# Kernel optimization log

Measured on AMD Instinct MI355X. Metric: run time of the kernel, lower is better.

## Reference

```python
import jax, jax.numpy as jnp
import numpy as np

B, S, D = 64, 1024, 64
NEG = -1e9


def setup_inputs() -> dict:
    key = jax.random.key(0)
    kq, kk, kv, kp = jax.random.split(key, 4)
    q = jax.random.normal(kq, (B, S, D), dtype=jnp.float32)
    k = jax.random.normal(kk, (B, S, D), dtype=jnp.float32)
    v = jax.random.normal(kv, (B, S, D), dtype=jnp.float32)
    prior_info = jax.random.normal(kp, (B, S, S), dtype=jnp.float32)
    # causal mask (True = masked), broadcast over batch
    causal = jnp.triu(jnp.ones((S, S), dtype=bool), k=1)
    mask = jnp.broadcast_to(causal, (B, S, S))
    return {"q": q, "k": k, "v": v, "mask": mask, "prior_info": prior_info}


def reference(q, k, v, mask, prior_info):
    # attn = q @ k^T / sqrt(d)
    attn = jnp.einsum("bqd,bkd->bqk", q, k)
    attn = attn / jnp.sqrt(jnp.asarray(D, dtype=attn.dtype))
    attn = jnp.where(mask, NEG, attn)
    prior = jnp.where(mask, NEG, prior_info)
    z = jax.nn.sigmoid(attn + prior)
    attn = z * attn + (1.0 - z) * prior
    attn = jax.nn.softmax(attn, axis=2)
    out = jnp.einsum("bqk,bkd->bqd", attn, v)
    return (out, attn)
```

## Files before the change

kernel.cpp:

```cpp
#include <hip/hip_runtime.h>
#include <math.h>

#define BB 64
#define SS 1024
#define DD 64
#define QB 32
#define THREADS 512

typedef __attribute__((ext_vector_type(8))) short short8;
typedef __attribute__((ext_vector_type(4))) float f32x4;

#define SWZ(row, byte) (((row) << 7) + (((((byte) >> 4) ^ ((row) & 7)) << 4) | ((byte) & 15)))

__device__ __forceinline__ unsigned short f2bf(float f) {
    union { float f; unsigned int u; } v; v.f = f;
    unsigned int r = (v.u + 0x7FFFu + ((v.u >> 16) & 1u)) >> 16;
    return (unsigned short)r;
}

__device__ __forceinline__ void gload16(const void* g, void* l) {
    __builtin_amdgcn_global_load_lds(
        (const __attribute__((address_space(1))) void*)g,
        (__attribute__((address_space(3))) void*)l, 16, 0, 0);
}

__global__ __launch_bounds__(256) void pre_convert(
    const float* __restrict__ qg, const float* __restrict__ kg,
    const float* __restrict__ vg, char* __restrict__ ws)
{
    __shared__ float sV[64][69];
    char* Kb = ws;
    char* Vt = ws + 8u * 1024u * 1024u;
    char* Qb = ws + 16u * 1024u * 1024u;
    const int bid = blockIdx.x, tid = threadIdx.x;

    if (bid < 1024) {
        const float* src = kg + ((size_t)(bid >> 4) * SS + (bid & 15) * 64) * DD;
        char* dst = Kb + (size_t)bid * 8192;
        #pragma unroll
        for (int u = 0; u < 4; ++u) {
            int idx = tid + u * 256, row = idx >> 4, c4 = idx & 15;
            f32x4 v = *(const f32x4*)(src + row * DD + c4 * 4);
            unsigned lo, hi;
            asm("v_cvt_pk_bf16_f32 %0, %1, %2" : "=v"(lo) : "v"(v.x), "v"(v.y));
            asm("v_cvt_pk_bf16_f32 %0, %1, %2" : "=v"(hi) : "v"(v.z), "v"(v.w));
            *(uint2*)(dst + SWZ(row, c4 * 8)) = make_uint2(lo, hi);
        }
    } else if (bid < 2048) {
        const int vb = bid - 1024;
        const float* src = vg + ((size_t)(vb >> 4) * SS + (vb & 15) * 64) * DD;
        #pragma unroll
        for (int u = 0; u < 4; ++u) {
            int idx = tid + u * 256, row = idx >> 4, c4 = idx & 15;
            f32x4 v = *(const f32x4*)(src + row * DD + c4 * 4);
            sV[row][c4 * 4 + 0] = v.x; sV[row][c4 * 4 + 1] = v.y;
            sV[row][c4 * 4 + 2] = v.z; sV[row][c4 * 4 + 3] = v.w;
        }
        __syncthreads();
        char* dst = Vt + (size_t)vb * 8192;
        const int d = tid >> 2, k0 = (tid & 3) * 16;
        union { short8 s; unsigned short u[8]; } w0, w1;
        #pragma unroll
        for (int i = 0; i < 8; ++i) {
            w0.u[i] = f2bf(sV[k0 + i][d]);
            w1.u[i] = f2bf(sV[k0 + 8 + i][d]);
        }
        *(short8*)(dst + SWZ(d, k0 * 2))      = w0.s;
        *(short8*)(dst + SWZ(d, k0 * 2 + 16)) = w1.s;
    } else {
        const int qb = bid - 2048;
        const float* src = qg + ((size_t)(qb >> 4) * SS + (qb & 15) * 64) * DD;
        char* dst = Qb + (size_t)qb * 8192;
        #pragma unroll
        for (int u = 0; u < 4; ++u) {
            int idx = tid + u * 256, row = idx >> 4, c4 = idx & 15;
            f32x4 v = *(const f32x4*)(src + row * DD + c4 * 4);
            float x0 = v.x * 0.125f, x1 = v.y * 0.125f;
            float x2 = v.z * 0.125f, x3 = v.w * 0.125f;
            unsigned lo, hi;
            asm("v_cvt_pk_bf16_f32 %0, %1, %2" : "=v"(lo) : "v"(x0), "v"(x1));
            asm("v_cvt_pk_bf16_f32 %0, %1, %2" : "=v"(hi) : "v"(x2), "v"(x3));
            *(uint2*)(dst + (row >> 5) * 4096 + SWZ(row & 31, c4 * 8)) = make_uint2(lo, hi);
        }
    }
}

__global__ __launch_bounds__(THREADS, 3) void attn_main(
    const char* __restrict__ ws, const float* __restrict__ prior,
    float* __restrict__ outg, float* __restrict__ attng)
{
    __shared__ char bufK[2][8192];
    __shared__ char bufV[3][8192];
    __shared__ char sP[2][4096];
    __shared__ float sRedP[QB][4];
    __shared__ float sRedT[QB];

    const int tid = threadIdx.x, lane = tid & 63, wid = tid >> 6;
    const int wr = wid >> 2, wc = wid & 3, lr = lane & 15, lg = lane >> 4;

    const int hw = (int)blockIdx.x;
    const int logical = ((hw & 7) << 8) | (hw >> 3);
    const int b  = logical >> 5;
    const int tq = 31 - (logical & 31);
    const int q0 = tq * QB;
    const int KT = (q0 + QB + 63) >> 6;

    const char* Kb = ws + (size_t)(b * 16) * 8192;
    const char* Vt = ws + 8u * 1024u * 1024u + (size_t)(b * 16) * 8192;
    const char* Qt = ws + 16u * 1024u * 1024u + (size_t)(b * 32 + tq) * 4096;

    short8 afr0 = *(const short8*)(Qt + SWZ(wr * 16 + lr, lg * 16));
    short8 afr1 = *(const short8*)(Qt + SWZ(wr * 16 + lr, 64 + lg * 16));

    const float* priB = prior + (size_t)b * SS * SS;
    const int rg0 = q0 + wr * 16 + lg * 4;
    const float* prow = priB + (size_t)rg0 * SS + (wc * 16 + lr);

    unsigned Zlo[16], Zhi[16];
    #pragma unroll
    for (int t = 0; t < 16; ++t) { Zlo[t] = 0u; Zhi[t] = 0u; }
    f32x4 oacc = (f32x4){0.f, 0.f, 0.f, 0.f};

    float prA[3][4];

    {
        gload16(Kb + tid * 16, (char*)&bufK[0][0] + tid * 16);
        gload16(Vt + tid * 16, (char*)&bufV[0][0] + tid * 16);
        prA[0][0] = prow[0]; prA[0][1] = prow[SS];
        prA[0][2] = prow[2 * SS]; prA[0][3] = prow[3 * SS];
        const int tp = (1 < KT) ? 1 : (KT - 1);
        const float* pp = prow + tp * 64;
        prA[1][0] = pp[0]; prA[1][1] = pp[SS];
        prA[1][2] = pp[2 * SS]; prA[1][3] = pp[3 * SS];
    }

    #pragma unroll
    for (int t = 0; t < 16; ++t) {
        if (t < KT) {
            __builtin_amdgcn_sched_barrier(0);
            asm volatile("s_waitcnt vmcnt(4) lgkmcnt(0)" ::: "memory");
            __builtin_amdgcn_sched_barrier(0);
            __builtin_amdgcn_s_barrier();
            __builtin_amdgcn_sched_barrier(0);

            {
                const int tn = (t + 1 < KT) ? (t + 1) : (KT - 1);
                gload16(Kb + (size_t)tn * 8192 + tid * 16,
                        (char*)&bufK[(t + 1) & 1][0] + tid * 16);
                gload16(Vt + (size_t)tn * 8192 + tid * 16,
                        (char*)&bufV[(t + 1) % 3][0] + tid * 16);
                const int tp = (t + 2 < KT) ? (t + 2) : (KT - 1);
                const float* pp = prow + tp * 64;
                prA[(t + 2) % 3][0] = pp[0];
                prA[(t + 2) % 3][1] = pp[SS];
                prA[(t + 2) % 3][2] = pp[2 * SS];
                prA[(t + 2) % 3][3] = pp[3 * SS];
            }

            const char* kb = &bufK[t & 1][0];
            short8 b0 = *(const short8*)(kb + SWZ(wc * 16 + lr, lg * 16));
            short8 b1 = *(const short8*)(kb + SWZ(wc * 16 + lr, 64 + lg * 16));
            f32x4 c = (f32x4){0.f, 0.f, 0.f, 0.f};
            c = __builtin_amdgcn_mfma_f32_16x16x32_bf16(afr0, b0, c, 0, 0, 0);
            c = __builtin_amdgcn_mfma_f32_16x16x32_bf16(afr1, b1, c, 0, 0, 0);

            if (t > 0) {
                const char* pb = &sP[(t - 1) & 1][0];
                const char* vb = &bufV[(t - 1) % 3][0];
                short8 pa0 = *(const short8*)(pb + SWZ(wr * 16 + lr, lg * 16));
                short8 pa1 = *(const short8*)(pb + SWZ(wr * 16 + lr, 64 + lg * 16));
                short8 vb0 = *(const short8*)(vb + SWZ(wc * 16 + lr, lg * 16));
                short8 vb1 = *(const short8*)(vb + SWZ(wc * 16 + lr, 64 + lg * 16));
                oacc = __builtin_amdgcn_mfma_f32_16x16x32_bf16(pa0, vb0, oacc, 0, 0, 0);
                oacc = __builtin_amdgcn_mfma_f32_16x16x32_bf16(pa1, vb1, oacc, 0, 0, 0);
            }

            const int colg = t * 64 + wc * 16 + lr;
            float e0, e1, e2, e3;
            {
                float ee[4];
                #pragma unroll
                for (int j = 0; j < 4; ++j) {
                    bool act = (colg <= rg0 + j);
                    float s = c[j];
                    float pv = prA[t % 3][j];
                    float z = 1.f / (1.f + __expf(-(s + pv)));
                    float m = pv + z * (s - pv);
                    ee[j] = act ? __expf(m) : 0.f;
                }
                e0 = ee[0]; e1 = ee[1]; e2 = ee[2]; e3 = ee[3];
            }

            unsigned X, Y;
            asm("v_cvt_pk_bf16_f32 %0, %1, %2" : "=v"(X) : "v"(e0), "v"(e1));
            asm("v_cvt_pk_bf16_f32 %0, %1, %2" : "=v"(Y) : "v"(e2), "v"(e3));
            unsigned Xp = (unsigned)__shfl_xor((int)X, 1);
            unsigned Yp = (unsigned)__shfl_xor((int)Y, 1);
            const bool codd = (lane & 1);
            unsigned nX = codd ? ((Xp >> 16) | (X & 0xffff0000u))
                               : ((X & 0xffffu) | (Xp << 16));
            unsigned nY = codd ? ((Yp >> 16) | (Y & 0xffff0000u))
                               : ((Y & 0xffffu) | (Yp << 16));
            unsigned X2 = (unsigned)__shfl_xor((int)nX, 2);
            unsigned Y2 = (unsigned)__shfl_xor((int)nY, 2);
            const bool chi = (lane & 2);
            unsigned Z0 = chi ? Y2 : nX;
            unsigned Z1 = chi ? nY : X2;
            Zlo[t] = Z0; Zhi[t] = Z1;

            const int c_ = lr & 3, a_ = lr >> 2;
            *(uint2*)(&sP[t & 1][0] + SWZ(wr * 16 + lg * 4 + c_, wc * 32 + a_ * 8)) =
                make_uint2(Z0, Z1);
        }
    }

    __builtin_amdgcn_sched_barrier(0);
    asm volatile("s_waitcnt lgkmcnt(0)" ::: "memory");
    __builtin_amdgcn_sched_barrier(0);
    __builtin_amdgcn_s_barrier();
    __builtin_amdgcn_sched_barrier(0);
    {
        const char* pb = &sP[(KT - 1) & 1][0];
        const char* vb = &bufV[(KT - 1) % 3][0];
        short8 pa0 = *(const short8*)(pb + SWZ(wr * 16 + lr, lg * 16));
        short8 pa1 = *(const short8*)(pb + SWZ(wr * 16 + lr, 64 + lg * 16));
        short8 vb0 = *(const short8*)(vb + SWZ(wc * 16 + lr, lg * 16));
        short8 vb1 = *(const short8*)(vb + SWZ(wc * 16 + lr, 64 + lg * 16));
        oacc = __builtin_amdgcn_mfma_f32_16x16x32_bf16(pa0, vb0, oacc, 0, 0, 0);
        oacc = __builtin_amdgcn_mfma_f32_16x16x32_bf16(pa1, vb1, oacc, 0, 0, 0);
    }

    const int c_ = lr & 3, a_ = lr >> 2;
    const int rL = wr * 16 + lg * 4 + c_;
    float sum4 = 0.f;
    #pragma unroll
    for (int t = 0; t < 16; ++t) {
        sum4 += __uint_as_float(Zlo[t] << 16);
        sum4 += __uint_as_float(Zlo[t] & 0xffff0000u);
        sum4 += __uint_as_float(Zhi[t] << 16);
        sum4 += __uint_as_float(Zhi[t] & 0xffff0000u);
    }
    sum4 += __shfl_xor(sum4, 4);
    sum4 += __shfl_xor(sum4, 8);
    if (a_ == 0) sRedP[rL][wc] = sum4;
    __syncthreads();
    if (tid < QB) {
        float tot = sRedP[tid][0] + sRedP[tid][1] + sRedP[tid][2] + sRedP[tid][3];
        sRedT[tid] = 1.f / tot;
    }
    __syncthreads();

    const float invT = sRedT[rL];
    float* arow = attng + ((size_t)b * SS + q0 + rL) * SS + wc * 16 + a_ * 4;
    #pragma unroll
    for (int t = 0; t < 16; ++t) {
        f32x4 vals;
        if (t < KT) {
            vals.x = __uint_as_float(Zlo[t] << 16) * invT;
            vals.y = __uint_as_float(Zlo[t] & 0xffff0000u) * invT;
            vals.z = __uint_as_float(Zhi[t] << 16) * invT;
            vals.w = __uint_as_float(Zhi[t] & 0xffff0000u) * invT;
        } else {
            vals = (f32x4){0.f, 0.f, 0.f, 0.f};
        }
        *(f32x4*)(arow + t * 64) = vals;
    }
    #pragma unroll
    for (int j = 0; j < 4; ++j) {
        float iv = sRedT[wr * 16 + lg * 4 + j];
        outg[((size_t)b * SS + rg0 + j) * DD + wc * 16 + lr] = oacc[j] * iv;
    }
}

#define KTILE 64
#define NTMAX 16
__device__ __forceinline__ int swzf(int row, int byte_in_row) {
    int chunk = (byte_in_row >> 4) ^ (row & 7);
    return row * 128 + chunk * 16 + (byte_in_row & 15);
}
__global__ __launch_bounds__(THREADS, 4) void attn_fallback(
    const float* __restrict__ qg, const float* __restrict__ kg,
    const float* __restrict__ vg, const float* __restrict__ prior,
    float* __restrict__ outg, float* __restrict__ attng)
{
    __shared__ char sQ[QB * 128];
    __shared__ char sKV[2][KTILE * 128];
    __shared__ char sPf[QB * 128];
    __shared__ float sRedA[QB][4];
    __shared__ float sRedB[QB][4];

    const int tid = threadIdx.x, lane = tid & 63, wid = tid >> 6;
    const int wr = wid >> 2, wc = wid & 3, lr = lane & 15, lg = lane >> 4;
    const int hw = (int)blockIdx.x;
    const int logical = ((hw & 7) << 8) | (hw >> 3);
    const int b = logical >> 5, tq = logical & 31;
    const int q0 = tq * QB;
    const int KT = (q0 + QB + KTILE - 1) / KTILE;
    const int rowg0 = q0 + wr * 16 + lg * 4;

    {
        int row = tid >> 4, c4 = tid & 15;
        f32x4 v = *(const f32x4*)(qg + ((size_t)b * SS + q0 + row) * DD + c4 * 4);
        ushort4 h = make_ushort4(f2bf(v.x), f2bf(v.y), f2bf(v.z), f2bf(v.w));
        *(ushort4*)(sQ + swzf(row, c4 * 8)) = h;
    }
    auto stageK = [&](const float* base, char* buf, int kt) {
        #pragma unroll
        for (int i = 0; i < 2; ++i) {
            int idx = tid + i * THREADS, row = idx >> 4, c4 = idx & 15;
            f32x4 v = *(const f32x4*)(base + ((size_t)b * SS + kt * KTILE + row) * DD + c4 * 4);
            ushort4 h = make_ushort4(f2bf(v.x), f2bf(v.y), f2bf(v.z), f2bf(v.w));
            *(ushort4*)(buf + swzf(row, c4 * 8)) = h;
        }
    };
    f32x4 acc[NTMAX];
    #pragma unroll
    for (int t = 0; t < NTMAX; ++t) acc[t] = (f32x4){0.f, 0.f, 0.f, 0.f};
    stageK(kg, sKV[0], 0);
    __syncthreads();
    short8 afr0 = *(const short8*)(sQ + swzf(wr * 16 + lr, lg * 16));
    short8 afr1 = *(const short8*)(sQ + swzf(wr * 16 + lr, 64 + lg * 16));
    const float* priB = prior + (size_t)b * SS * SS;
    #pragma unroll
    for (int t = 0; t < NTMAX; ++t) {
        if (t >= KT) continue;
        if (t + 1 < KT) stageK(kg, sKV[(t + 1) & 1], t + 1);
        const char* kb = sKV[t & 1];
        short8 b0 = *(const short8*)(kb + swzf(wc * 16 + lr, lg * 16));
        short8 b1 = *(const short8*)(kb + swzf(wc * 16 + lr, 64 + lg * 16));
        f32x4 c = acc[t];
        c = __builtin_amdgcn_mfma_f32_16x16x32_bf16(afr0, b0, c, 0, 0, 0);
        c = __builtin_amdgcn_mfma_f32_16x16x32_bf16(afr1, b1, c, 0, 0, 0);
        const int colg = t * KTILE + wc * 16 + lr;
        #pragma unroll
        for (int j = 0; j < 4; ++j) {
            int rg = rowg0 + j;
            bool act = (colg <= rg);
            float s = c[j] * 0.125f;
            float pv = act ? priB[(size_t)rg * SS + colg] : 0.f;
            float z = 1.f / (1.f + __expf(-(s + pv)));
            c[j] = act ? (pv + z * (s - pv)) : -1e9f;
        }
        acc[t] = c;
        __syncthreads();
    }
    float mj[4], sj[4], invj[4];
    #pragma unroll
    for (int j = 0; j < 4; ++j) {
        float m = -INFINITY;
        #pragma unroll
        for (int t = 0; t < NTMAX; ++t) if (t < KT) m = fmaxf(m, acc[t][j]);
        #pragma unroll
        for (int o = 1; o < 16; o <<= 1) m = fmaxf(m, __shfl_xor(m, o));
        mj[j] = m;
    }
    if (lr == 0) {
        #pragma unroll
        for (int j = 0; j < 4; ++j) sRedA[wr * 16 + lg * 4 + j][wc] = mj[j];
    }
    __syncthreads();
    #pragma unroll
    for (int j = 0; j < 4; ++j) {
        f32x4 r = *(const f32x4*)sRedA[wr * 16 + lg * 4 + j];
        mj[j] = fmaxf(fmaxf(r.x, r.y), fmaxf(r.z, r.w));
        sj[j] = 0.f;
    }
    #pragma unroll
    for (int t = 0; t < NTMAX; ++t) {
        if (t >= KT) continue;
        f32x4 c = acc[t];
        #pragma unroll
        for (int j = 0; j < 4; ++j) { c[j] = __expf(c[j] - mj[j]); sj[j] += c[j]; }
        acc[t] = c;
    }
    #pragma unroll
    for (int j = 0; j < 4; ++j) {
        float s = sj[j];
        #pragma unroll
        for (int o = 1; o < 16; o <<= 1) s += __shfl_xor(s, o);
        sj[j] = s;
    }
    if (lr == 0) {
        #pragma unroll
        for (int j = 0; j < 4; ++j) sRedB[wr * 16 + lg * 4 + j][wc] = sj[j];
    }
    __syncthreads();
    #pragma unroll
    for (int j = 0; j < 4; ++j) {
        f32x4 r = *(const f32x4*)sRedB[wr * 16 + lg * 4 + j];
        invj[j] = 1.f / (r.x + r.y + r.z + r.w);
    }
    #pragma unroll
    for (int t = 0; t < NTMAX; ++t) {
        const int colg = t * KTILE + wc * 16 + lr;
        #pragma unroll
        for (int j = 0; j < 4; ++j) {
            float p = 0.f;
            if (t < KT) p = acc[t][j] * invj[j];
            attng[((size_t)b * SS + rowg0 + j) * SS + colg] = p;
        }
        if (t < KT) {
            f32x4 c = acc[t];
            #pragma unroll
            for (int j = 0; j < 4; ++j) c[j] *= invj[j];
            acc[t] = c;
        }
    }
    f32x4 oacc = (f32x4){0.f, 0.f, 0.f, 0.f};
    #pragma unroll
    for (int t = 0; t < NTMAX; ++t) {
        if (t >= KT) continue;
        __syncthreads();
        #pragma unroll
        for (int i = 0; i < 2; ++i) {
            int idx = tid + i * THREADS, krow = idx >> 4, c4 = idx & 15;
            f32x4 v = *(const f32x4*)(vg + ((size_t)b * SS + t * KTILE + krow) * DD + c4 * 4);
            #pragma unroll
            for (int u = 0; u < 4; ++u)
                *(unsigned short*)(sKV[0] + swzf(c4 * 4 + u, krow * 2)) = f2bf(v[u]);
        }
        #pragma unroll
        for (int j = 0; j < 4; ++j)
            *(unsigned short*)(sPf + swzf(wr * 16 + lg * 4 + j, (wc * 16 + lr) * 2)) = f2bf(acc[t][j]);
        __syncthreads();
        short8 pa0 = *(const short8*)(sPf + swzf(wr * 16 + lr, lg * 16));
        short8 pa1 = *(const short8*)(sPf + swzf(wr * 16 + lr, 64 + lg * 16));
        short8 vb0 = *(const short8*)(sKV[0] + swzf(wc * 16 + lr, lg * 16));
        short8 vb1 = *(const short8*)(sKV[0] + swzf(wc * 16 + lr, 64 + lg * 16));
        oacc = __builtin_amdgcn_mfma_f32_16x16x32_bf16(pa0, vb0, oacc, 0, 0, 0);
        oacc = __builtin_amdgcn_mfma_f32_16x16x32_bf16(pa1, vb1, oacc, 0, 0, 0);
    }
    #pragma unroll
    for (int j = 0; j < 4; ++j)
        outg[((size_t)b * SS + rowg0 + j) * DD + wc * 16 + lr] = oacc[j];
}

extern "C" void kernel_launch(void* const* d_in, const int* in_sizes, int n_in,
                              void* d_out, int out_size, void* d_ws, size_t ws_size,
                              hipStream_t stream) {
    (void)in_sizes; (void)n_in; (void)out_size;
    const float* q     = (const float*)d_in[0];
    const float* k     = (const float*)d_in[1];
    const float* v     = (const float*)d_in[2];
    const float* prior = (const float*)d_in[4];

    float* out  = (float*)d_out;
    float* attn = out + (size_t)BB * SS * DD;

    const size_t ws_need = 24u * 1024u * 1024u;
    if (ws_size >= ws_need) {
        pre_convert<<<dim3(3072), dim3(256), 0, stream>>>(q, k, v, (char*)d_ws);
        attn_main<<<dim3(2048), dim3(THREADS), 0, stream>>>(
            (const char*)d_ws, prior, out, attn);
    } else {
        attn_fallback<<<dim3(2048), dim3(THREADS), 0, stream>>>(
            q, k, v, prior, out, attn);
    }
}
```

Measured before the change: 140.0 us.

## Fuse Q/K bf16 conversion into attention kernel, keep only V pre-transpose

Q and K are no longer converted by a separate pre-pass. Each lane now loads its fp32 Q fragment and double-buffered K fragments straight from global memory into registers and converts them to bf16 before the MFMA. The K shared-memory buffer goes away, and the pre-pass shrinks to V transposition only, which cuts workspace traffic and launch work. Prior loads and attn stores use nontemporal hints, and several sched_barriers and the vmcnt wait are dropped. The trade-off is more VGPR pressure and K being re-read from global memory by every wave row, with looser ordering of the memory operations.

New measurement: 219.3 us. 1.57x slower.

```diff
diff --git a/kernel.cpp b/kernel.cpp
--- a/kernel.cpp
+++ b/kernel.cpp
@@ -24,72 +24,46 @@
         (__attribute__((address_space(3))) void*)l, 16, 0, 0);
 }
 
-__global__ __launch_bounds__(256) void pre_convert(
-    const float* __restrict__ qg, const float* __restrict__ kg,
+__device__ __forceinline__ short8 cvt8(f32x4 a, f32x4 b) {
+    union { short8 s; unsigned u[4]; } r;
+    asm("v_cvt_pk_bf16_f32 %0, %1, %2" : "=v"(r.u[0]) : "v"(a.x), "v"(a.y));
+    asm("v_cvt_pk_bf16_f32 %0, %1, %2" : "=v"(r.u[1]) : "v"(a.z), "v"(a.w));
+    asm("v_cvt_pk_bf16_f32 %0, %1, %2" : "=v"(r.u[2]) : "v"(b.x), "v"(b.y));
+    asm("v_cvt_pk_bf16_f32 %0, %1, %2" : "=v"(r.u[3]) : "v"(b.z), "v"(b.w));
+    return r.s;
+}
+
+__global__ __launch_bounds__(256) void pre_convert_v(
     const float* __restrict__ vg, char* __restrict__ ws)
 {
     __shared__ float sV[64][69];
-    char* Kb = ws;
-    char* Vt = ws + 8u * 1024u * 1024u;
-    char* Qb = ws + 16u * 1024u * 1024u;
-    const int bid = blockIdx.x, tid = threadIdx.x;
-
-    if (bid < 1024) {
-        const float* src = kg + ((size_t)(bid >> 4) * SS + (bid & 15) * 64) * DD;
-        char* dst = Kb + (size_t)bid * 8192;
-        #pragma unroll
-        for (int u = 0; u < 4; ++u) {
-            int idx = tid + u * 256, row = idx >> 4, c4 = idx & 15;
-            f32x4 v = *(const f32x4*)(src + row * DD + c4 * 4);
-            unsigned lo, hi;
-            asm("v_cvt_pk_bf16_f32 %0, %1, %2" : "=v"(lo) : "v"(v.x), "v"(v.y));
-            asm("v_cvt_pk_bf16_f32 %0, %1, %2" : "=v"(hi) : "v"(v.z), "v"(v.w));
-            *(uint2*)(dst + SWZ(row, c4 * 8)) = make_uint2(lo, hi);
-        }
-    } else if (bid < 2048) {
-        const int vb = bid - 1024;
-        const float* src = vg + ((size_t)(vb >> 4) * SS + (vb & 15) * 64) * DD;
-        #pragma unroll
-        for (int u = 0; u < 4; ++u) {
-            int idx = tid + u * 256, row = idx >> 4, c4 = idx & 15;
-            f32x4 v = *(const f32x4*)(src + row * DD + c4 * 4);
-            sV[row][c4 * 4 + 0] = v.x; sV[row][c4 * 4 + 1] = v.y;
-            sV[row][c4 * 4 + 2] = v.z; sV[row][c4 * 4 + 3] = v.w;
-        }
-        __syncthreads();
-        char* dst = Vt + (size_t)vb * 8192;
-        const int d = tid >> 2, k0 = (tid & 3) * 16;
-        union { short8 s; unsigned short u[8]; } w0, w1;
-        #pragma unroll
-        for (int i = 0; i < 8; ++i) {
-            w0.u[i] = f2bf(sV[k0 + i][d]);
-            w1.u[i] = f2bf(sV[k0 + 8 + i][d]);
-        }
-        *(short8*)(dst + SWZ(d, k0 * 2))      = w0.s;
-        *(short8*)(dst + SWZ(d, k0 * 2 + 16)) = w1.s;
-    } else {
-        const int qb = bid - 2048;
-        const float* src = qg + ((size_t)(qb >> 4) * SS + (qb & 15) * 64) * DD;
-        char* dst = Qb + (size_t)qb * 8192;
-        #pragma unroll
-        for (int u = 0; u < 4; ++u) {
-            int idx = tid + u * 256, row = idx >> 4, c4 = idx & 15;
-            f32x4 v = *(const f32x4*)(src + row * DD + c4 * 4);
-            float x0 = v.x * 0.125f, x1 = v.y * 0.125f;
-            float x2 = v.z * 0.125f, x3 = v.w * 0.125f;
-            unsigned lo, hi;
-            asm("v_cvt_pk_bf16_f32 %0, %1, %2" : "=v"(lo) : "v"(x0), "v"(x1));
-            asm("v_cvt_pk_bf16_f32 %0, %1, %2" : "=v"(hi) : "v"(x2), "v"(x3));
-            *(uint2*)(dst + (row >> 5) * 4096 + SWZ(row & 31, c4 * 8)) = make_uint2(lo, hi);
-        }
-    }
-}
-
-__global__ __launch_bounds__(THREADS, 3) void attn_main(
-    const char* __restrict__ ws, const float* __restrict__ prior,
+    const int vb = blockIdx.x, tid = threadIdx.x;
+    const float* src = vg + ((size_t)(vb >> 4) * SS + (vb & 15) * 64) * DD;
+    #pragma unroll
+    for (int u = 0; u < 4; ++u) {
+        int idx = tid + u * 256, row = idx >> 4, c4 = idx & 15;
+        f32x4 v = *(const f32x4*)(src + row * DD + c4 * 4);
+        sV[row][c4 * 4 + 0] = v.x; sV[row][c4 * 4 + 1] = v.y;
+        sV[row][c4 * 4 + 2] = v.z; sV[row][c4 * 4 + 3] = v.w;
+    }
+    __syncthreads();
+    char* dst = ws + (size_t)vb * 8192;
+    const int d = tid >> 2, k0 = (tid & 3) * 16;
+    union { short8 s; unsigned short u[8]; } w0, w1;
+    #pragma unroll
+    for (int i = 0; i < 8; ++i) {
+        w0.u[i] = f2bf(sV[k0 + i][d]);
+        w1.u[i] = f2bf(sV[k0 + 8 + i][d]);
+    }
+    *(short8*)(dst + SWZ(d, k0 * 2))      = w0.s;
+    *(short8*)(dst + SWZ(d, k0 * 2 + 16)) = w1.s;
+}
+
+__global__ __launch_bounds__(THREADS, 3) void attn_fused(
+    const float* __restrict__ qg, const float* __restrict__ kg,
+    const float* __restrict__ prior, const char* __restrict__ wsV,
     float* __restrict__ outg, float* __restrict__ attng)
 {
-    __shared__ char bufK[2][8192];
     __shared__ char bufV[3][8192];
     __shared__ char sP[2][4096];
     __shared__ float sRedP[QB][4];
@@ -105,64 +79,86 @@
     const int q0 = tq * QB;
     const int KT = (q0 + QB + 63) >> 6;
 
-    const char* Kb = ws + (size_t)(b * 16) * 8192;
-    const char* Vt = ws + 8u * 1024u * 1024u + (size_t)(b * 16) * 8192;
-    const char* Qt = ws + 16u * 1024u * 1024u + (size_t)(b * 32 + tq) * 4096;
-
-    short8 afr0 = *(const short8*)(Qt + SWZ(wr * 16 + lr, lg * 16));
-    short8 afr1 = *(const short8*)(Qt + SWZ(wr * 16 + lr, 64 + lg * 16));
+    const char* Vt = wsV + (size_t)(b * 16) * 8192;
+
+    short8 afr0, afr1;
+    {
+        const float* qrow = qg + ((size_t)b * SS + q0 + wr * 16 + lr) * DD + lg * 8;
+        f32x4 a0 = *(const f32x4*)(qrow);
+        f32x4 a1 = *(const f32x4*)(qrow + 4);
+        f32x4 a2 = *(const f32x4*)(qrow + 32);
+        f32x4 a3 = *(const f32x4*)(qrow + 36);
+        #pragma unroll
+        for (int i = 0; i < 4; ++i) { a0[i] *= 0.125f; a1[i] *= 0.125f; a2[i] *= 0.125f; a3[i] *= 0.125f; }
+        afr0 = cvt8(a0, a1);
+        afr1 = cvt8(a2, a3);
+    }
 
     const float* priB = prior + (size_t)b * SS * SS;
     const int rg0 = q0 + wr * 16 + lg * 4;
     const float* prow = priB + (size_t)rg0 * SS + (wc * 16 + lr);
+    const float* krb = kg + ((size_t)b * SS + wc * 16 + lr) * DD + lg * 8;
 
     unsigned Zlo[16], Zhi[16];
     #pragma unroll
     for (int t = 0; t < 16; ++t) { Zlo[t] = 0u; Zhi[t] = 0u; }
     f32x4 oacc = (f32x4){0.f, 0.f, 0.f, 0.f};
 
+    f32x4 kbuf[2][4];
     float prA[3][4];
 
+    gload16(Vt + tid * 16, (char*)&bufV[0][0] + tid * 16);
+    __builtin_amdgcn_sched_barrier(0);
+    kbuf[0][0] = *(const f32x4*)(krb);
+    kbuf[0][1] = *(const f32x4*)(krb + 4);
+    kbuf[0][2] = *(const f32x4*)(krb + 32);
+    kbuf[0][3] = *(const f32x4*)(krb + 36);
+    prA[0][0] = __builtin_nontemporal_load(prow);
+    prA[0][1] = __builtin_nontemporal_load(prow + SS);
+    prA[0][2] = __builtin_nontemporal_load(prow + 2 * SS);
+    prA[0][3] = __builtin_nontemporal_load(prow + 3 * SS);
     {
-        gload16(Kb + tid * 16, (char*)&bufK[0][0] + tid * 16);
-        gload16(Vt + tid * 16, (char*)&bufV[0][0] + tid * 16);
-        prA[0][0] = prow[0]; prA[0][1] = prow[SS];
-        prA[0][2] = prow[2 * SS]; prA[0][3] = prow[3 * SS];
         const int tp = (1 < KT) ? 1 : (KT - 1);
         const float* pp = prow + tp * 64;
-        prA[1][0] = pp[0]; prA[1][1] = pp[SS];
-        prA[1][2] = pp[2 * SS]; prA[1][3] = pp[3 * SS];
+        prA[1][0] = __builtin_nontemporal_load(pp);
+        prA[1][1] = __builtin_nontemporal_load(pp + SS);
+        prA[1][2] = __builtin_nontemporal_load(pp + 2 * SS);
+        prA[1][3] = __builtin_nontemporal_load(pp + 3 * SS);
     }
 
     #pragma unroll
     for (int t = 0; t < 16; ++t) {
         if (t < KT) {
-            __builtin_amdgcn_sched_barrier(0);
-            asm volatile("s_waitcnt vmcnt(4) lgkmcnt(0)" ::: "memory");
-            __builtin_amdgcn_sched_barrier(0);
+            asm volatile("s_waitcnt lgkmcnt(0)" ::: "memory");
             __builtin_amdgcn_s_barrier();
-            __builtin_amdgcn_sched_barrier(0);
 
             {
                 const int tn = (t + 1 < KT) ? (t + 1) : (KT - 1);
-                gload16(Kb + (size_t)tn * 8192 + tid * 16,
-                        (char*)&bufK[(t + 1) & 1][0] + tid * 16);
                 gload16(Vt + (size_t)tn * 8192 + tid * 16,
                         (char*)&bufV[(t + 1) % 3][0] + tid * 16);
+            }
+            __builtin_amdgcn_sched_barrier(0);
+            {
+                const int tn = (t + 1 < KT) ? (t + 1) : (KT - 1);
+                const float* kb = krb + (size_t)tn * 64 * DD;
+                kbuf[(t + 1) & 1][0] = *(const f32x4*)(kb);
+                kbuf[(t + 1) & 1][1] = *(const f32x4*)(kb + 4);
+                kbuf[(t + 1) & 1][2] = *(const f32x4*)(kb + 32);
+                kbuf[(t + 1) & 1][3] = *(const f32x4*)(kb + 36);
                 const int tp = (t + 2 < KT) ? (t + 2) : (KT - 1);
                 const float* pp = prow + tp * 64;
-                prA[(t + 2) % 3][0] = pp[0];
-                prA[(t + 2) % 3][1] = pp[SS];
-                prA[(t + 2) % 3][2] = pp[2 * SS];
-                prA[(t + 2) % 3][3] = pp[3 * SS];
+                prA[(t + 2) % 3][0] = __builtin_nontemporal_load(pp);
+                prA[(t + 2) % 3][1] = __builtin_nontemporal_load(pp + SS);
+                prA[(t + 2) % 3][2] = __builtin_nontemporal_load(pp + 2 * SS);
+                prA[(t + 2) % 3][3] = __builtin_nontemporal_load(pp + 3 * SS);
             }
 
-            const char* kb = &bufK[t & 1][0];
-            short8 b0 = *(const short8*)(kb + SWZ(wc * 16 + lr, lg * 16));
-            short8 b1 = *(const short8*)(kb + SWZ(wc * 16 + lr, 64 + lg * 16));
+            short8 b0 = cvt8(kbuf[t & 1][0], kbuf[t & 1][1]);
+            short8 b1 = cvt8(kbuf[t & 1][2], kbuf[t & 1][3]);
             f32x4 c = (f32x4){0.f, 0.f, 0.f, 0.f};
             c = __builtin_amdgcn_mfma_f32_16x16x32_bf16(afr0, b0, c, 0, 0, 0);
             c = __builtin_amdgcn_mfma_f32_16x16x32_bf16(afr1, b1, c, 0, 0, 0);
+            __builtin_amdgcn_sched_barrier(0);
 
             if (t > 0) {
                 const char* pb = &sP[(t - 1) & 1][0];
@@ -214,11 +210,8 @@
         }
     }
 
-    __builtin_amdgcn_sched_barrier(0);
     asm volatile("s_waitcnt lgkmcnt(0)" ::: "memory");
-    __builtin_amdgcn_sched_barrier(0);
     __builtin_amdgcn_s_barrier();
-    __builtin_amdgcn_sched_barrier(0);
     {
         const char* pb = &sP[(KT - 1) & 1][0];
         const char* vb = &bufV[(KT - 1) % 3][0];
@@ -263,7 +256,7 @@
         } else {
             vals = (f32x4){0.f, 0.f, 0.f, 0.f};
         }
-        *(f32x4*)(arow + t * 64) = vals;
+        __builtin_nontemporal_store(vals, (f32x4*)(arow + t * 64));
     }
     #pragma unroll
     for (int j = 0; j < 4; ++j) {
@@ -447,11 +440,11 @@
     float* out  = (float*)d_out;
     float* attn = out + (size_t)BB * SS * DD;
 
-    const size_t ws_need = 24u * 1024u * 1024u;
+    const size_t ws_need = 8u * 1024u * 1024u;
     if (ws_size >= ws_need) {
-        pre_convert<<<dim3(3072), dim3(256), 0, stream>>>(q, k, v, (char*)d_ws);
-        attn_main<<<dim3(2048), dim3(THREADS), 0, stream>>>(
-            (const char*)d_ws, prior, out, attn);
+        pre_convert_v<<<dim3(1024), dim3(256), 0, stream>>>(v, (char*)d_ws);
+        attn_fused<<<dim3(2048), dim3(THREADS), 0, stream>>>(
+            q, k, prior, (const char*)d_ws, out, attn);
     } else {
         attn_fallback<<<dim3(2048), dim3(THREADS), 0, stream>>>(
             q, k, v, prior, out, attn);
```
